# Optimization experiments

Measured on AMD Instinct MI355X. Metric: run time of the kernel, lower is better.

## Reference

```python
import jax, jax.numpy as jnp
import numpy as np

B, C, H, IN = 128, 1024, 256, 19  # batch, subcarriers, hidden, input dim
P = 2 * H                          # prism input dim (att + rad features)
NL = 8                             # layers in attenuation/radiance nets
UEBS = 2 * 4                       # num_ue_antennas * num_bs_antennas


def _init(key, shape, scale=0.02):
    return (jax.random.normal(key, shape, dtype=jnp.float32) * scale)


def setup_inputs() -> dict:
    key = jax.random.key(0)
    ks = jax.random.split(key, 24)
    return {
        "positions": jax.random.normal(ks[0], (B, 3), dtype=jnp.float32),
        "ue_antennas": jax.random.normal(ks[1], (B, 2), dtype=jnp.float32),
        "bs_antennas": jax.random.normal(ks[2], (B, 4), dtype=jnp.float32),
        "additional_features": jax.random.normal(ks[3], (B, 10), dtype=jnp.float32),
        "att_W1": _init(ks[4], (IN, H)), "att_b1": _init(ks[5], (H,)),
        "att_Wh": _init(ks[6], (NL - 1, H, H)), "att_bh": _init(ks[7], (NL - 1, H)),
        # radiance net: same structure
        "rad_W1": _init(ks[8], (IN, H)), "rad_b1": _init(ks[9], (H,)),
        "rad_Wh": _init(ks[10], (NL - 1, H, H)), "rad_bh": _init(ks[11], (NL - 1, H)),
        # RF prism: per-subcarrier stacked weights
        "prism_W1": _init(ks[12], (C, P, H)), "prism_b1": _init(ks[13], (C, H)),
        "prism_W2": _init(ks[14], (C, H, H)), "prism_b2": _init(ks[15], (C, H)),
        "prism_W3": _init(ks[16], (C, H)), "prism_b3": _init(ks[17], (C,)),
        # mimo head: Linear(1 -> ue*bs)
        "mimo_W": _init(ks[18], (1, UEBS)), "mimo_b": _init(ks[19], (UEBS,)),
    }


def _deep_mlp(x, W1, b1, Wh, bh):
    h = jax.nn.relu(x @ W1 + b1)
    def step(h, wb):
        W, b = wb
        return jax.nn.relu(h @ W + b), None
    h, _ = jax.lax.scan(step, h, (Wh, bh))
    return h


def reference(positions, ue_antennas, bs_antennas, additional_features,
              att_W1, att_b1, att_Wh, att_bh,
              rad_W1, rad_b1, rad_Wh, rad_bh,
              prism_W1, prism_b1, prism_W2, prism_b2, prism_W3, prism_b3,
              mimo_W, mimo_b):
    x = jnp.concatenate([positions, ue_antennas, bs_antennas, additional_features], axis=1)  # [B,19]
    att = _deep_mlp(x, att_W1, att_b1, att_Wh, att_bh)  # [B,H]
    rad = _deep_mlp(x, rad_W1, rad_b1, rad_Wh, rad_bh)  # [B,H]
    feat = jnp.concatenate([att, rad], axis=1)  # [B,2H]
    # batched per-subcarrier 3-layer MLPs (grouped GEMMs)
    h1 = jax.nn.relu(jnp.einsum('bi,cio->bco', feat, prism_W1) + prism_b1)  # [B,C,H]
    h2 = jax.nn.relu(jnp.einsum('bch,cho->bco', h1, prism_W2) + prism_b2)   # [B,C,H]
    sub = jnp.einsum('bch,ch->bc', h2, prism_W3) + prism_b3                 # [B,C]
    mimo = sub.mean(axis=1, keepdims=True) @ mimo_W + mimo_b                # [B,8]
    return sub, mimo
```

## Files before the change

kernel.cpp:

```cpp
#include <hip/hip_runtime.h>
#include <hip/hip_bf16.h>
#include <stdint.h>

#define Bv 128
#define Hv 256
#define INv 19
#define Pv 512
#define Cv 1024
#define NLh 7
#define CH 32

typedef __attribute__((ext_vector_type(4))) float floatx4;
typedef __attribute__((ext_vector_type(8))) short shortx8;
typedef __attribute__((ext_vector_type(4))) unsigned int uintx4;

__device__ __forceinline__ unsigned int cvt_pk_bf16(float lo, float hi) {
    unsigned int r;
    asm("v_cvt_pk_bf16_f32 %0, %1, %2" : "=v"(r) : "v"(lo), "v"(hi));
    return r;
}

__device__ __forceinline__ int swz(int r) { return ((r & 7) ^ ((r >> 3) & 7)); }

__global__ __launch_bounds__(256) void mlp_fused(
    const float* __restrict__ pos, const float* __restrict__ ue,
    const float* __restrict__ bs,  const float* __restrict__ addf,
    const float* __restrict__ attW1, const float* __restrict__ attb1,
    const float* __restrict__ attWh, const float* __restrict__ attbh,
    const float* __restrict__ radW1, const float* __restrict__ radb1,
    const float* __restrict__ radWh, const float* __restrict__ radbh,
    unsigned short* __restrict__ feat)
{
    int blk = blockIdx.x;
    int net = blk >> 6, bq = blk & 63;
    const float* W1 = net ? radW1 : attW1;
    const float* b1 = net ? radb1 : attb1;
    const float* Wh = net ? radWh : attWh;
    const float* bh = net ? radbh : attbh;
    __shared__ float xs[2][INv];
    __shared__ float hr[2][Hv];
    __shared__ float part[4][2][Hv];
    int t = threadIdx.x;
    if (t < 2 * INv) {
        int r = t / INv, k = t - r * INv;
        int b = bq * 2 + r;
        float v;
        if (k < 3) v = pos[b*3 + k];
        else if (k < 5) v = ue[b*2 + (k-3)];
        else if (k < 9) v = bs[b*4 + (k-5)];
        else v = addf[b*10 + (k-9)];
        xs[r][k] = v;
    }
    __syncthreads();
    {
        float a0 = b1[t], a1 = a0;
        #pragma unroll
        for (int k = 0; k < INv; ++k) {
            float w = W1[k*Hv + t];
            a0 += xs[0][k] * w;
            a1 += xs[1][k] * w;
        }
        hr[0][t] = fmaxf(a0, 0.f);
        hr[1][t] = fmaxf(a1, 0.f);
    }
    __syncthreads();
    int half = t >> 6, oq = t & 63;
    for (int layer = 0; layer < NLh; ++layer) {
        const float* W = Wh + (size_t)layer * Hv * Hv;
        const float* Wp = W + (size_t)(half * 64) * Hv + oq * 4;
        floatx4 a0r0 = {0.f,0.f,0.f,0.f}, a1r0 = {0.f,0.f,0.f,0.f};
        floatx4 a0r1 = {0.f,0.f,0.f,0.f}, a1r1 = {0.f,0.f,0.f,0.f};
        #pragma unroll 8
        for (int kk = 0; kk < 64; kk += 2) {
            floatx4 w0 = *reinterpret_cast<const floatx4*>(Wp + (size_t)kk * Hv);
            floatx4 w1 = *reinterpret_cast<const floatx4*>(Wp + (size_t)(kk+1) * Hv);
            float h00 = hr[0][half*64 + kk], h01 = hr[0][half*64 + kk + 1];
            float h10 = hr[1][half*64 + kk], h11 = hr[1][half*64 + kk + 1];
            a0r0 += w0 * h00; a1r0 += w1 * h01;
            a0r1 += w0 * h10; a1r1 += w1 * h11;
        }
        floatx4 r0 = a0r0 + a1r0, r1 = a0r1 + a1r1;
        *reinterpret_cast<floatx4*>(&part[half][0][oq*4]) = r0;
        *reinterpret_cast<floatx4*>(&part[half][1][oq*4]) = r1;
        __syncthreads();
        int r = t >> 7, o2 = (t & 127) * 2;
        const float* bias = bh + layer * Hv;
        float s0 = part[0][r][o2]   + part[1][r][o2]   + part[2][r][o2]   + part[3][r][o2]   + bias[o2];
        float s1 = part[0][r][o2+1] + part[1][r][o2+1] + part[2][r][o2+1] + part[3][r][o2+1] + bias[o2+1];
        s0 = fmaxf(s0, 0.f); s1 = fmaxf(s1, 0.f);
        if (layer == NLh - 1) {
            *reinterpret_cast<unsigned int*>(
                feat + (size_t)(bq*2 + r) * Pv + net*Hv + o2) = cvt_pk_bf16(s0, s1);
        } else {
            hr[r][o2] = s0; hr[r][o2+1] = s1;
        }
        __syncthreads();
    }
}


__device__ __forceinline__ void dma16(const float* g, char* lds) {
    __builtin_amdgcn_global_load_lds(
        (const __attribute__((address_space(1))) unsigned int*)g,
        (__attribute__((address_space(3))) unsigned int*)lds, 16, 0, 0);
}

__device__ __forceinline__ void dma_chunk(const float* csrc, char* buf, int w, int l) {
    #pragma unroll
    for (int i = 0; i < 4; ++i) {
        int k = w * 4 + i;
        int perm = ((k >> 3) & 3) << 3;
        dma16(csrc + (size_t)k * Hv + ((l * 4) ^ perm), buf + k * 1024);
    }
}

__device__ __forceinline__ shortx8 bfrag(const char* buf, int o, int l) {
    const int kb = (l >> 4) * 8;
    const int col = o ^ (((l >> 4) & 3) << 3);
    const char* p = buf + kb * 1024 + col * 4;
    float a0 = *(const float*)(p + 0*1024);
    float a1 = *(const float*)(p + 1*1024);
    float a2 = *(const float*)(p + 2*1024);
    float a3 = *(const float*)(p + 3*1024);
    float a4 = *(const float*)(p + 4*1024);
    float a5 = *(const float*)(p + 5*1024);
    float a6 = *(const float*)(p + 6*1024);
    float a7 = *(const float*)(p + 7*1024);
    uintx4 v = { cvt_pk_bf16(a0, a1), cvt_pk_bf16(a2, a3),
                 cvt_pk_bf16(a4, a5), cvt_pk_bf16(a6, a7) };
    shortx8 r;
    __builtin_memcpy(&r, &v, 16);
    return r;
}

__device__ __forceinline__ void stage_af(const unsigned short* __restrict__ feat,
                                         int u, int wm, int l, shortx8* a) {
    #pragma unroll
    for (int m = 0; m < 4; ++m) {
        int row = wm*64 + m*16 + (l & 15);
        a[m] = *reinterpret_cast<const shortx8*>(
            feat + (size_t)row * Pv + u*CH + ((l >> 4) & 3) * 8);
    }
}


__global__ __launch_bounds__(512, 1) void prism_kernel(
    const unsigned short* __restrict__ feat,
    const float* __restrict__ W1, const float* __restrict__ b1,
    const float* __restrict__ W2, const float* __restrict__ b2,
    const float* __restrict__ W3, const float* __restrict__ b3,
    float* __restrict__ out)
{
    __shared__ __align__(16) char smem[163840];
    char* wb0 = smem;
    char* wb1 = smem + 32768;
    char* wb2 = smem + 65536;
    char* h1  = smem + 98304;
    float* subws = (float*)(smem + 98304);

    const int tid = threadIdx.x;
    const int l = tid & 63;
    const int w = tid >> 6;
    const int wm = w >> 2, wn = w & 3;
    const int c = blockIdx.x;
    const float* W1c = W1 + (size_t)c * (Pv * Hv);
    const float* W2c = W2 + (size_t)c * (Hv * Hv);

    shortx8 arr0[4], arr1[4];

    stage_af(feat, 0, wm, l, arr0);
    __builtin_amdgcn_sched_barrier(0);
    dma_chunk(W1c, wb0, w, l);
    __builtin_amdgcn_sched_barrier(0);
    stage_af(feat, 1, wm, l, arr1);
    __builtin_amdgcn_sched_barrier(0);
    dma_chunk(W1c + (size_t)1 * CH * Hv, wb1, w, l);
    dma_chunk(W1c + (size_t)2 * CH * Hv, wb2, w, l);
    asm volatile("s_waitcnt vmcnt(12)" ::: "memory");
    __builtin_amdgcn_sched_barrier(0);
    __builtin_amdgcn_s_barrier();

    floatx4 acc[4][4];
    #pragma unroll
    for (int m = 0; m < 4; ++m)
        #pragma unroll
        for (int n = 0; n < 4; ++n)
            acc[m][n] = (floatx4){0.f, 0.f, 0.f, 0.f};

    #pragma unroll
    for (int u = 0; u < 16; ++u) {
        if (u >= 1 && u + 1 < 16)
            stage_af(feat, u + 1, wm, l, ((u + 1) & 1) ? arr1 : arr0);
        __builtin_amdgcn_sched_barrier(0);
        if (u >= 1) {
            const float* ps = (u + 2 < 16) ? W1c + (size_t)(u + 2) * CH * Hv
                                           : W2c + (size_t)(u + 2 - 16) * CH * Hv;
            char* dst = ((u + 2) % 3 == 0) ? wb0 : ((u + 2) % 3 == 1) ? wb1 : wb2;
            dma_chunk(ps, dst, w, l);
        }
        __builtin_amdgcn_sched_barrier(0);
        {
            const char* buf = (u % 3 == 0) ? wb0 : (u % 3 == 1) ? wb1 : wb2;
            const shortx8* ac = (u & 1) ? arr1 : arr0;
            #pragma unroll
            for (int n = 0; n < 4; ++n) {
                int o = wn*64 + n*16 + (l & 15);
                shortx8 bf = bfrag(buf, o, l);
                #pragma unroll
                for (int m = 0; m < 4; ++m)
                    acc[m][n] = __builtin_amdgcn_mfma_f32_16x16x32_bf16(ac[m], bf, acc[m][n], 0, 0, 0);
            }
        }
        asm volatile("s_waitcnt vmcnt(4) lgkmcnt(0)" ::: "memory");
        __builtin_amdgcn_sched_barrier(0);
        __builtin_amdgcn_s_barrier();
    }

    {
        float bias1v[4];
        #pragma unroll
        for (int n = 0; n < 4; ++n)
            bias1v[n] = b1[c*Hv + wn*64 + n*16 + (l & 15)];
        #pragma unroll
        for (int m = 0; m < 4; ++m) {
            #pragma unroll
            for (int n = 0; n < 4; ++n) {
                int o = wn*64 + n*16 + (l & 15);
                #pragma unroll
                for (int jj = 0; jj < 4; ++jj) {
                    int bb = wm*64 + m*16 + (l >> 4)*4 + jj;
                    float v = fmaxf(acc[m][n][jj] + bias1v[n], 0.f);
                    *(unsigned short*)(h1 + bb*512 + ((o*2) ^ (swz(bb) << 4))) =
                        (unsigned short)(cvt_pk_bf16(v, v) & 0xffffu);
                }
            }
        }
    }
    asm volatile("s_waitcnt lgkmcnt(0)" ::: "memory");
    __builtin_amdgcn_s_barrier();

    #pragma unroll
    for (int m = 0; m < 4; ++m)
        #pragma unroll
        for (int n = 0; n < 4; ++n)
            acc[m][n] = (floatx4){0.f, 0.f, 0.f, 0.f};

    #pragma unroll
    for (int u = 16; u < 24; ++u) {
        if (u + 2 < 24) {
            char* dst = ((u + 2) % 3 == 0) ? wb0 : ((u + 2) % 3 == 1) ? wb1 : wb2;
            dma_chunk(W2c + (size_t)(u + 2 - 16) * CH * Hv, dst, w, l);
        }
        __builtin_amdgcn_sched_barrier(0);
        {
            const char* buf = (u % 3 == 0) ? wb0 : (u % 3 == 1) ? wb1 : wb2;
            int k2 = (u - 16) * CH + (l >> 4) * 8;
            shortx8 af[4];
            #pragma unroll
            for (int m = 0; m < 4; ++m) {
                int row = wm*64 + m*16 + (l & 15);
                af[m] = *reinterpret_cast<const shortx8*>(
                    h1 + row*512 + ((k2*2) ^ (swz(row) << 4)));
            }
            #pragma unroll
            for (int n = 0; n < 4; ++n) {
                int o = wn*64 + n*16 + (l & 15);
                shortx8 bf = bfrag(buf, o, l);
                #pragma unroll
                for (int m = 0; m < 4; ++m)
                    acc[m][n] = __builtin_amdgcn_mfma_f32_16x16x32_bf16(af[m], bf, acc[m][n], 0, 0, 0);
            }
        }
        if (u < 22) asm volatile("s_waitcnt vmcnt(4) lgkmcnt(0)" ::: "memory");
        else        asm volatile("s_waitcnt vmcnt(0) lgkmcnt(0)" ::: "memory");
        __builtin_amdgcn_sched_barrier(0);
        __builtin_amdgcn_s_barrier();
    }

    float bias2v[4], w3v[4];
    #pragma unroll
    for (int n = 0; n < 4; ++n) {
        int o = wn*64 + n*16 + (l & 15);
        bias2v[n] = b2[c*Hv + o];
        w3v[n]    = W3[c*Hv + o];
    }
    float b3v = b3[c];
    float p[4][4];
    #pragma unroll
    for (int m = 0; m < 4; ++m)
        #pragma unroll
        for (int jj = 0; jj < 4; ++jj) {
            float s = 0.f;
            #pragma unroll
            for (int n = 0; n < 4; ++n)
                s += fmaxf(acc[m][n][jj] + bias2v[n], 0.f) * w3v[n];
            p[m][jj] = s;
        }
    #pragma unroll
    for (int m = 0; m < 4; ++m)
        #pragma unroll
        for (int jj = 0; jj < 4; ++jj) {
            p[m][jj] += __shfl_xor(p[m][jj], 1, 64);
            p[m][jj] += __shfl_xor(p[m][jj], 2, 64);
            p[m][jj] += __shfl_xor(p[m][jj], 4, 64);
            p[m][jj] += __shfl_xor(p[m][jj], 8, 64);
        }
    {
        int t16 = l & 15;
        float pv = 0.f;
        #pragma unroll
        for (int m = 0; m < 4; ++m)
            #pragma unroll
            for (int jj = 0; jj < 4; ++jj)
                if (m == (t16 >> 2) && jj == (t16 & 3)) pv = p[m][jj];
        int bb = wm*64 + (t16 >> 2)*16 + (l >> 4)*4 + (t16 & 3);
        subws[wn*128 + bb] = pv;
    }
    asm volatile("s_waitcnt lgkmcnt(0)" ::: "memory");
    __builtin_amdgcn_s_barrier();
    if (tid < 128) {
        float s = subws[tid] + subws[128 + tid] + subws[256 + tid] + subws[384 + tid] + b3v;
        out[(size_t)tid * Cv + c] = s;
    }
}


__global__ __launch_bounds__(256) void mimo_kernel(
    const float* __restrict__ sub, const float* __restrict__ mW,
    const float* __restrict__ mB, float* __restrict__ out)
{
    int b = blockIdx.x;
    int t = threadIdx.x;
    float s = 0.f;
    #pragma unroll
    for (int j = 0; j < 4; ++j) s += sub[b*Cv + t + j*256];
    #pragma unroll
    for (int m = 1; m < 64; m <<= 1) s += __shfl_xor(s, m, 64);
    __shared__ float red[4];
    if ((t & 63) == 0) red[t >> 6] = s;
    __syncthreads();
    if (t < 8) {
        float mean = (red[0] + red[1] + red[2] + red[3]) * (1.0f / 1024.0f);
        out[Bv * Cv + b*8 + t] = mean * mW[t] + mB[t];
    }
}


extern "C" void kernel_launch(void* const* d_in, const int* in_sizes, int n_in,
                              void* d_out, int out_size, void* d_ws, size_t ws_size,
                              hipStream_t stream) {
    (void)in_sizes; (void)n_in; (void)out_size; (void)ws_size;
    const float* pos   = (const float*)d_in[0];
    const float* ue    = (const float*)d_in[1];
    const float* bsant = (const float*)d_in[2];
    const float* addf  = (const float*)d_in[3];
    const float* attW1 = (const float*)d_in[4];
    const float* attb1 = (const float*)d_in[5];
    const float* attWh = (const float*)d_in[6];
    const float* attbh = (const float*)d_in[7];
    const float* radW1 = (const float*)d_in[8];
    const float* radb1 = (const float*)d_in[9];
    const float* radWh = (const float*)d_in[10];
    const float* radbh = (const float*)d_in[11];
    const float* pW1   = (const float*)d_in[12];
    const float* pb1   = (const float*)d_in[13];
    const float* pW2   = (const float*)d_in[14];
    const float* pb2   = (const float*)d_in[15];
    const float* pW3   = (const float*)d_in[16];
    const float* pb3   = (const float*)d_in[17];
    const float* mW    = (const float*)d_in[18];
    const float* mB    = (const float*)d_in[19];
    float* out = (float*)d_out;

    unsigned short* feat = (unsigned short*)d_ws;

    mlp_fused<<<128, 256, 0, stream>>>(pos, ue, bsant, addf,
                                       attW1, attb1, attWh, attbh,
                                       radW1, radb1, radWh, radbh, feat);
    prism_kernel<<<Cv, 512, 0, stream>>>(feat, pW1, pb1, pW2, pb2, pW3, pb3, out);
    mimo_kernel<<<Bv, 256, 0, stream>>>(out, mW, mB, out);
}
```

Measured before the change: 225.9 us.

## Load prism weights directly from global into registers, drop LDS DMA pipeline

```diff
diff --git a/kernel.cpp b/kernel.cpp
--- a/kernel.cpp
+++ b/kernel.cpp
@@ -8,7 +8,6 @@
 #define Pv 512
 #define Cv 1024
 #define NLh 7
-#define CH 32
 
 typedef __attribute__((ext_vector_type(4))) float floatx4;
 typedef __attribute__((ext_vector_type(8))) short shortx8;
@@ -21,6 +20,9 @@
 }
 
 __device__ __forceinline__ int swz(int r) { return ((r & 7) ^ ((r >> 3) & 7)); }
+
+#define BAR() do { asm volatile("s_waitcnt lgkmcnt(0)" ::: "memory"); \
+                   __builtin_amdgcn_s_barrier(); } while (0)
 
 __global__ __launch_bounds__(256) void mlp_fused(
     const float* __restrict__ pos, const float* __restrict__ ue,
@@ -99,50 +101,17 @@
 }
 
 
-__device__ __forceinline__ void dma16(const float* g, char* lds) {
-    __builtin_amdgcn_global_load_lds(
-        (const __attribute__((address_space(1))) unsigned int*)g,
-        (__attribute__((address_space(3))) unsigned int*)lds, 16, 0, 0);
-}
-
-__device__ __forceinline__ void dma_chunk(const float* csrc, char* buf, int w, int l) {
-    #pragma unroll
-    for (int i = 0; i < 4; ++i) {
-        int k = w * 4 + i;
-        int perm = ((k >> 3) & 3) << 3;
-        dma16(csrc + (size_t)k * Hv + ((l * 4) ^ perm), buf + k * 1024);
-    }
-}
-
-__device__ __forceinline__ shortx8 bfrag(const char* buf, int o, int l) {
-    const int kb = (l >> 4) * 8;
-    const int col = o ^ (((l >> 4) & 3) << 3);
-    const char* p = buf + kb * 1024 + col * 4;
-    float a0 = *(const float*)(p + 0*1024);
-    float a1 = *(const float*)(p + 1*1024);
-    float a2 = *(const float*)(p + 2*1024);
-    float a3 = *(const float*)(p + 3*1024);
-    float a4 = *(const float*)(p + 4*1024);
-    float a5 = *(const float*)(p + 5*1024);
-    float a6 = *(const float*)(p + 6*1024);
-    float a7 = *(const float*)(p + 7*1024);
+__device__ __forceinline__ shortx8 wfrag(const float* __restrict__ Wc,
+                                         int kbase, int o, int l) {
+    const float* p = Wc + (size_t)(kbase + (l >> 4) * 8) * Hv + o + (l & 15);
+    float a0 = p[0*Hv], a1 = p[1*Hv], a2 = p[2*Hv], a3 = p[3*Hv];
+    float a4 = p[4*Hv], a5 = p[5*Hv], a6 = p[6*Hv], a7 = p[7*Hv];
     uintx4 v = { cvt_pk_bf16(a0, a1), cvt_pk_bf16(a2, a3),
                  cvt_pk_bf16(a4, a5), cvt_pk_bf16(a6, a7) };
     shortx8 r;
     __builtin_memcpy(&r, &v, 16);
     return r;
 }
-
-__device__ __forceinline__ void stage_af(const unsigned short* __restrict__ feat,
-                                         int u, int wm, int l, shortx8* a) {
-    #pragma unroll
-    for (int m = 0; m < 4; ++m) {
-        int row = wm*64 + m*16 + (l & 15);
-        a[m] = *reinterpret_cast<const shortx8*>(
-            feat + (size_t)row * Pv + u*CH + ((l >> 4) & 3) * 8);
-    }
-}
-
 
 __global__ __launch_bounds__(512, 1) void prism_kernel(
     const unsigned short* __restrict__ feat,
@@ -151,175 +120,120 @@
     const float* __restrict__ W3, const float* __restrict__ b3,
     float* __restrict__ out)
 {
-    __shared__ __align__(16) char smem[163840];
-    char* wb0 = smem;
-    char* wb1 = smem + 32768;
-    char* wb2 = smem + 65536;
-    char* h1  = smem + 98304;
-    float* subws = (float*)(smem + 98304);
+    __shared__ __align__(16) char h1[65536];
+    __shared__ float subws[8 * Bv];
 
     const int tid = threadIdx.x;
     const int l = tid & 63;
     const int w = tid >> 6;
-    const int wm = w >> 2, wn = w & 3;
     const int c = blockIdx.x;
+    const int ob = w * 32;
     const float* W1c = W1 + (size_t)c * (Pv * Hv);
     const float* W2c = W2 + (size_t)c * (Hv * Hv);
 
-    shortx8 arr0[4], arr1[4];
-
-    stage_af(feat, 0, wm, l, arr0);
-    __builtin_amdgcn_sched_barrier(0);
-    dma_chunk(W1c, wb0, w, l);
-    __builtin_amdgcn_sched_barrier(0);
-    stage_af(feat, 1, wm, l, arr1);
-    __builtin_amdgcn_sched_barrier(0);
-    dma_chunk(W1c + (size_t)1 * CH * Hv, wb1, w, l);
-    dma_chunk(W1c + (size_t)2 * CH * Hv, wb2, w, l);
-    asm volatile("s_waitcnt vmcnt(12)" ::: "memory");
-    __builtin_amdgcn_sched_barrier(0);
-    __builtin_amdgcn_s_barrier();
-
-    floatx4 acc[4][4];
-    #pragma unroll
-    for (int m = 0; m < 4; ++m)
-        #pragma unroll
-        for (int n = 0; n < 4; ++n)
-            acc[m][n] = (floatx4){0.f, 0.f, 0.f, 0.f};
+    floatx4 acc[8][2];
+    #pragma unroll
+    for (int m = 0; m < 8; ++m) {
+        acc[m][0] = (floatx4){0.f, 0.f, 0.f, 0.f};
+        acc[m][1] = (floatx4){0.f, 0.f, 0.f, 0.f};
+    }
 
     #pragma unroll
     for (int u = 0; u < 16; ++u) {
-        if (u >= 1 && u + 1 < 16)
-            stage_af(feat, u + 1, wm, l, ((u + 1) & 1) ? arr1 : arr0);
-        __builtin_amdgcn_sched_barrier(0);
-        if (u >= 1) {
-            const float* ps = (u + 2 < 16) ? W1c + (size_t)(u + 2) * CH * Hv
-                                           : W2c + (size_t)(u + 2 - 16) * CH * Hv;
-            char* dst = ((u + 2) % 3 == 0) ? wb0 : ((u + 2) % 3 == 1) ? wb1 : wb2;
-            dma_chunk(ps, dst, w, l);
-        }
-        __builtin_amdgcn_sched_barrier(0);
-        {
-            const char* buf = (u % 3 == 0) ? wb0 : (u % 3 == 1) ? wb1 : wb2;
-            const shortx8* ac = (u & 1) ? arr1 : arr0;
-            #pragma unroll
-            for (int n = 0; n < 4; ++n) {
-                int o = wn*64 + n*16 + (l & 15);
-                shortx8 bf = bfrag(buf, o, l);
-                #pragma unroll
-                for (int m = 0; m < 4; ++m)
-                    acc[m][n] = __builtin_amdgcn_mfma_f32_16x16x32_bf16(ac[m], bf, acc[m][n], 0, 0, 0);
-            }
-        }
-        asm volatile("s_waitcnt vmcnt(4) lgkmcnt(0)" ::: "memory");
-        __builtin_amdgcn_sched_barrier(0);
-        __builtin_amdgcn_s_barrier();
+        shortx8 af[8];
+        #pragma unroll
+        for (int m = 0; m < 8; ++m) {
+            int row = m * 16 + (l & 15);
+            af[m] = *reinterpret_cast<const shortx8*>(
+                feat + (size_t)row * Pv + u * 32 + (l >> 4) * 8);
+        }
+        shortx8 bf0 = wfrag(W1c, u * 32, ob, l);
+        shortx8 bf1 = wfrag(W1c, u * 32, ob + 16, l);
+        #pragma unroll
+        for (int m = 0; m < 8; ++m) {
+            acc[m][0] = __builtin_amdgcn_mfma_f32_16x16x32_bf16(af[m], bf0, acc[m][0], 0, 0, 0);
+            acc[m][1] = __builtin_amdgcn_mfma_f32_16x16x32_bf16(af[m], bf1, acc[m][1], 0, 0, 0);
+        }
     }
 
     {
-        float bias1v[4];
-        #pragma unroll
-        for (int n = 0; n < 4; ++n)
-            bias1v[n] = b1[c*Hv + wn*64 + n*16 + (l & 15)];
-        #pragma unroll
-        for (int m = 0; m < 4; ++m) {
-            #pragma unroll
-            for (int n = 0; n < 4; ++n) {
-                int o = wn*64 + n*16 + (l & 15);
+        float bias1v[2] = { b1[c*Hv + ob + (l & 15)], b1[c*Hv + ob + 16 + (l & 15)] };
+        #pragma unroll
+        for (int m = 0; m < 8; ++m) {
+            #pragma unroll
+            for (int n = 0; n < 2; ++n) {
+                int o = ob + n * 16 + (l & 15);
                 #pragma unroll
                 for (int jj = 0; jj < 4; ++jj) {
-                    int bb = wm*64 + m*16 + (l >> 4)*4 + jj;
+                    int row = m * 16 + (l >> 4) * 4 + jj;
                     float v = fmaxf(acc[m][n][jj] + bias1v[n], 0.f);
-                    *(unsigned short*)(h1 + bb*512 + ((o*2) ^ (swz(bb) << 4))) =
+                    *(unsigned short*)(h1 + row*512 + ((o*2) ^ (swz(row) << 4))) =
                         (unsigned short)(cvt_pk_bf16(v, v) & 0xffffu);
                 }
             }
         }
     }
-    asm volatile("s_waitcnt lgkmcnt(0)" ::: "memory");
-    __builtin_amdgcn_s_barrier();
-
-    #pragma unroll
-    for (int m = 0; m < 4; ++m)
-        #pragma unroll
-        for (int n = 0; n < 4; ++n)
-            acc[m][n] = (floatx4){0.f, 0.f, 0.f, 0.f};
-
-    #pragma unroll
-    for (int u = 16; u < 24; ++u) {
-        if (u + 2 < 24) {
-            char* dst = ((u + 2) % 3 == 0) ? wb0 : ((u + 2) % 3 == 1) ? wb1 : wb2;
-            dma_chunk(W2c + (size_t)(u + 2 - 16) * CH * Hv, dst, w, l);
-        }
-        __builtin_amdgcn_sched_barrier(0);
-        {
-            const char* buf = (u % 3 == 0) ? wb0 : (u % 3 == 1) ? wb1 : wb2;
-            int k2 = (u - 16) * CH + (l >> 4) * 8;
-            shortx8 af[4];
-            #pragma unroll
-            for (int m = 0; m < 4; ++m) {
-                int row = wm*64 + m*16 + (l & 15);
-                af[m] = *reinterpret_cast<const shortx8*>(
-                    h1 + row*512 + ((k2*2) ^ (swz(row) << 4)));
+    BAR();
+
+    #pragma unroll
+    for (int m = 0; m < 8; ++m) {
+        acc[m][0] = (floatx4){0.f, 0.f, 0.f, 0.f};
+        acc[m][1] = (floatx4){0.f, 0.f, 0.f, 0.f};
+    }
+
+    #pragma unroll
+    for (int u = 0; u < 8; ++u) {
+        shortx8 af[8];
+        #pragma unroll
+        for (int m = 0; m < 8; ++m) {
+            int row = m * 16 + (l & 15);
+            int k2 = u * 32 + (l >> 4) * 8;
+            af[m] = *reinterpret_cast<const shortx8*>(
+                h1 + row*512 + ((k2*2) ^ (swz(row) << 4)));
+        }
+        shortx8 bf0 = wfrag(W2c, u * 32, ob, l);
+        shortx8 bf1 = wfrag(W2c, u * 32, ob + 16, l);
+        #pragma unroll
+        for (int m = 0; m < 8; ++m) {
+            acc[m][0] = __builtin_amdgcn_mfma_f32_16x16x32_bf16(af[m], bf0, acc[m][0], 0, 0, 0);
+            acc[m][1] = __builtin_amdgcn_mfma_f32_16x16x32_bf16(af[m], bf1, acc[m][1], 0, 0, 0);
+        }
+    }
+
+    {
+        float bias2v[2] = { b2[c*Hv + ob + (l & 15)], b2[c*Hv + ob + 16 + (l & 15)] };
+        float w3v[2]    = { W3[c*Hv + ob + (l & 15)], W3[c*Hv + ob + 16 + (l & 15)] };
+        float p[8][4];
+        #pragma unroll
+        for (int m = 0; m < 8; ++m)
+            #pragma unroll
+            for (int jj = 0; jj < 4; ++jj) {
+                float s = fmaxf(acc[m][0][jj] + bias2v[0], 0.f) * w3v[0]
+                        + fmaxf(acc[m][1][jj] + bias2v[1], 0.f) * w3v[1];
+                p[m][jj] = s;
             }
-            #pragma unroll
-            for (int n = 0; n < 4; ++n) {
-                int o = wn*64 + n*16 + (l & 15);
-                shortx8 bf = bfrag(buf, o, l);
+        #pragma unroll
+        for (int m = 0; m < 8; ++m)
+            #pragma unroll
+            for (int jj = 0; jj < 4; ++jj) {
+                p[m][jj] += __shfl_xor(p[m][jj], 1, 64);
+                p[m][jj] += __shfl_xor(p[m][jj], 2, 64);
+                p[m][jj] += __shfl_xor(p[m][jj], 4, 64);
+                p[m][jj] += __shfl_xor(p[m][jj], 8, 64);
+            }
+        if ((l & 15) == 0) {
+            #pragma unroll
+            for (int m = 0; m < 8; ++m)
                 #pragma unroll
-                for (int m = 0; m < 4; ++m)
-                    acc[m][n] = __builtin_amdgcn_mfma_f32_16x16x32_bf16(af[m], bf, acc[m][n], 0, 0, 0);
-            }
-        }
-        if (u < 22) asm volatile("s_waitcnt vmcnt(4) lgkmcnt(0)" ::: "memory");
-        else        asm volatile("s_waitcnt vmcnt(0) lgkmcnt(0)" ::: "memory");
-        __builtin_amdgcn_sched_barrier(0);
-        __builtin_amdgcn_s_barrier();
-    }
-
-    float bias2v[4], w3v[4];
-    #pragma unroll
-    for (int n = 0; n < 4; ++n) {
-        int o = wn*64 + n*16 + (l & 15);
-        bias2v[n] = b2[c*Hv + o];
-        w3v[n]    = W3[c*Hv + o];
-    }
-    float b3v = b3[c];
-    float p[4][4];
-    #pragma unroll
-    for (int m = 0; m < 4; ++m)
-        #pragma unroll
-        for (int jj = 0; jj < 4; ++jj) {
-            float s = 0.f;
-            #pragma unroll
-            for (int n = 0; n < 4; ++n)
-                s += fmaxf(acc[m][n][jj] + bias2v[n], 0.f) * w3v[n];
-            p[m][jj] = s;
-        }
-    #pragma unroll
-    for (int m = 0; m < 4; ++m)
-        #pragma unroll
-        for (int jj = 0; jj < 4; ++jj) {
-            p[m][jj] += __shfl_xor(p[m][jj], 1, 64);
-            p[m][jj] += __shfl_xor(p[m][jj], 2, 64);
-            p[m][jj] += __shfl_xor(p[m][jj], 4, 64);
-            p[m][jj] += __shfl_xor(p[m][jj], 8, 64);
-        }
-    {
-        int t16 = l & 15;
-        float pv = 0.f;
-        #pragma unroll
-        for (int m = 0; m < 4; ++m)
-            #pragma unroll
-            for (int jj = 0; jj < 4; ++jj)
-                if (m == (t16 >> 2) && jj == (t16 & 3)) pv = p[m][jj];
-        int bb = wm*64 + (t16 >> 2)*16 + (l >> 4)*4 + (t16 & 3);
-        subws[wn*128 + bb] = pv;
-    }
-    asm volatile("s_waitcnt lgkmcnt(0)" ::: "memory");
-    __builtin_amdgcn_s_barrier();
-    if (tid < 128) {
-        float s = subws[tid] + subws[128 + tid] + subws[256 + tid] + subws[384 + tid] + b3v;
+                for (int jj = 0; jj < 4; ++jj)
+                    subws[w * Bv + m*16 + (l >> 4)*4 + jj] = p[m][jj];
+        }
+    }
+    BAR();
+    if (tid < Bv) {
+        float s = b3[c];
+        #pragma unroll
+        for (int ww = 0; ww < 8; ++ww) s += subws[ww * Bv + tid];
         out[(size_t)tid * Cv + c] = s;
     }
 }
```

Measured after the change: 352.4 us. 56.0% more time.
